# Kernel tuning notes

Hardware: AMD Instinct MI355X
Metric: run time of the kernel (lower is better)

The kernel has to match this reference:

```python
import jax, jax.numpy as jnp
import numpy as np

N, F, C, H, HX = 100000, 500, 40, 256, 64
E = 1_600_000


def setup_inputs() -> dict:
    key = jax.random.key(0)
    ks = jax.random.split(key, 12)
    s = lambda fan_in: 1.0 / np.sqrt(fan_in)
    return {
        "x": jax.random.normal(ks[0], (N, F), dtype=jnp.float32),
        "y": jax.random.randint(ks[1], (N,), 0, C),
        "train_mask": jax.random.randint(ks[2], (N,), 0, 2).astype(bool),
        "edge_index": jax.random.randint(ks[3], (2, E), 0, N),
        "edge_index_neg": jax.random.randint(ks[4], (2, E), 0, N),
        "fc1_w": jax.random.uniform(ks[5], (H, F), jnp.float32, -s(F), s(F)),
        "fc1_b": jnp.zeros((H,), jnp.float32),
        "fc2_w": jax.random.uniform(ks[6], (C, H), jnp.float32, -s(H), s(H)),
        "fc2_b": jnp.zeros((C,), jnp.float32),
        "xenc_w": jax.random.uniform(ks[7], (HX, F), jnp.float32, -s(F), s(F)),
        "xenc_b": jnp.zeros((HX,), jnp.float32),
        "pexy_w": jax.random.uniform(ks[8], (1, 2 * (HX + C)), jnp.float32, -s(2 * (HX + C)), s(2 * (HX + C))),
        "pexy_b": jnp.zeros((1,), jnp.float32),
    }


def reference(x, y, train_mask, edge_index, edge_index_neg,
              fc1_w, fc1_b, fc2_w, fc2_b, xenc_w, xenc_b, pexy_w, pexy_b):
    temperature = 1.0
    # MLP p(y|x), inference mode (dropout is identity)
    h = jax.nn.relu(x @ fc1_w.T + fc1_b)
    logits = (h @ fc2_w.T + fc2_b) / temperature
    y_log_prob = jax.nn.log_softmax(logits, axis=-1)            # [N, C]
    y_prob = jnp.exp(y_log_prob)
    one_hot = jax.nn.one_hot(y, y_prob.shape[1], dtype=y_prob.dtype)
    y_prob = jnp.where(train_mask[:, None], one_hot, y_prob)    # [N, C]

    # node encoder
    xe = jax.nn.relu(x @ xenc_w.T + xenc_b)                     # [N, HX]

    # The scorer Linear(2*(HX+C) -> 1) applied to cat([x_q, x_k, y_q, y_k])
    # decomposes into per-node query/key scalars (same math, no big concat):
    hx = xe.shape[1]
    w = pexy_w[0]
    w_xq, w_xk = w[:hx], w[hx:2 * hx]
    w_yq, w_yk = w[2 * hx:2 * hx + y_prob.shape[1]], w[2 * hx + y_prob.shape[1]:]
    s_q = xe @ w_xq + y_prob @ w_yq                             # [N]
    s_k = xe @ w_xk + y_prob @ w_yk                             # [N]

    def edge_scores(ei):
        return (s_q[ei[0]] + s_k[ei[1]] + pexy_b[0])[:, None]   # [E, 1]

    e_pred_pos = edge_scores(edge_index)
    e_pred_neg = edge_scores(edge_index_neg)
    return (e_pred_pos, e_pred_neg, y_log_prob)
```

## Files before the change

kernel.cpp:

```cpp
#include <hip/hip_runtime.h>
#include <stdint.h>

#define N_NODES 100000
#define F_DIM   500
#define C_DIM   40
#define H_DIM   256
#define HX_DIM  64
#define O_DIM   320
#define E_NUM   1600000

typedef unsigned short u16;
typedef unsigned int   u32;
typedef __attribute__((ext_vector_type(4))) u16    u16x4;
typedef __attribute__((ext_vector_type(8))) u16    u16x8;
typedef __attribute__((ext_vector_type(4))) float  f32x4;
typedef __attribute__((ext_vector_type(8))) short  bf16x8;

__device__ __forceinline__ float bf2f(u16 v) {
  u32 u = ((u32)v) << 16;
  return __builtin_bit_cast(float, u);
}
__device__ __forceinline__ u16 f2bf(float f) {
  u32 x = __builtin_bit_cast(u32, f);
  x += 0x7fffu + ((x >> 16) & 1u);
  return (u16)(x >> 16);
}

__global__ __launch_bounds__(256) void k_detect(const u32* __restrict__ tm, int* __restrict__ flag)
{
  __shared__ int s;
  if (threadIdx.x == 0) s = 0;
  __syncthreads();
  int local = 0;
  #pragma unroll
  for (int j = 0; j < 16; ++j) {
    if (tm[j * 256 + threadIdx.x] > 1u) local = 1;
  }
  if (local) s = 1;
  __syncthreads();
  if (threadIdx.x == 0) *flag = s;
}

__global__ __launch_bounds__(256) void k_cvtw(
    const float* __restrict__ fc1w, const float* __restrict__ xencw, u16* __restrict__ wws)
{
  const int g = blockIdx.x * 256 + threadIdx.x;
  const int c = g / 1280;
  const int rem = g - c * 1280;
  const int r = rem >> 2;
  const int k0 = c * 32 + (rem & 3) * 8;
  const float* src = (r < H_DIM) ? (fc1w + (long)r * F_DIM)
                                 : (xencw + (long)(r - H_DIM) * F_DIM);
  f32x4 v0 = {0.f, 0.f, 0.f, 0.f}, v1 = v0;
  if (k0 + 4 <= F_DIM) v0 = *(const f32x4*)(src + k0);
  if (k0 + 8 <= F_DIM) v1 = *(const f32x4*)(src + k0 + 4);
  u16x8 o;
  #pragma unroll
  for (int i = 0; i < 4; ++i) { o[i] = f2bf(v0[i]); o[4 + i] = f2bf(v1[i]); }
  *(u16x8*)(wws + (size_t)g * 8) = o;
}

__global__ __launch_bounds__(256) void k_cvtw2(
    const float* __restrict__ fc2w, const float* __restrict__ pw, u16* __restrict__ wwsB)
{
  const int g = blockIdx.x * 256 + threadIdx.x;
  if (g >= 1920) return;
  const int kc = g / 192;
  const int rem = g - kc * 192;
  const int r = rem >> 2;
  const int k0 = kc * 32 + (rem & 3) * 8;
  const float* src = nullptr;
  if (r < C_DIM)           { if (k0 + 8 <= H_DIM) src = fc2w + r * H_DIM + k0; }
  else if (r == C_DIM)     { if (k0 >= H_DIM) src = pw + (k0 - H_DIM); }
  else if (r == C_DIM + 1) { if (k0 >= H_DIM) src = pw + HX_DIM + (k0 - H_DIM); }
  u16x8 o = {0, 0, 0, 0, 0, 0, 0, 0};
  if (src) {
    const f32x4 v0 = *(const f32x4*)src;
    const f32x4 v1 = *(const f32x4*)(src + 4);
    #pragma unroll
    for (int i = 0; i < 4; ++i) { o[i] = f2bf(v0[i]); o[4 + i] = f2bf(v1[i]); }
  }
  *(u16x8*)(wwsB + (size_t)g * 8) = o;
}

#define BN   320
#define RH_LD 328

__global__ __launch_bounds__(256, 4) void k_fused(
    const float* __restrict__ x, const u16* __restrict__ wws, const u16* __restrict__ wwsB,
    const float* __restrict__ fc1b, const float* __restrict__ xencb,
    const int* __restrict__ y, const void* __restrict__ tmask,
    const float* __restrict__ fc2b, const float* __restrict__ pw,
    const int* __restrict__ mask_flag,
    float* __restrict__ out_lp, float* __restrict__ sq_out, float* __restrict__ sk_out)
{
  __shared__ __align__(16) u16 smem[16384];
  u16* sOut = smem;

  const int tid  = threadIdx.x;
  const int lane = tid & 63;
  const int wcol = tid >> 6;
  const int l15 = lane & 15, lgrp = lane >> 4;
  const long rowbase = (long)blockIdx.x * 32;

  {
    f32x4 v0[4], v1[4];
    #pragma unroll
    for (int half = 0; half < 2; ++half) {
      #pragma unroll
      for (int i = 0; i < 4; ++i) {
        const int g = tid + 256 * (half * 4 + i);
        const int r = g >> 6, c = g & 63;
        const int k0 = c * 8;
        v0[i] = (f32x4){0.f, 0.f, 0.f, 0.f};
        v1[i] = v0[i];
        const float* p = x + (rowbase + r) * F_DIM + k0;
        if (k0 + 4 <= F_DIM) v0[i] = *(const f32x4*)p;
        if (k0 + 8 <= F_DIM) v1[i] = *(const f32x4*)(p + 4);
      }
      #pragma unroll
      for (int i = 0; i < 4; ++i) {
        const int g = tid + 256 * (half * 4 + i);
        const int r = g >> 6, c = g & 63;
        const int phys = c ^ (r & 7);
        u16x8 o;
        #pragma unroll
        for (int j = 0; j < 4; ++j) { o[j] = f2bf(v0[i][j]); o[4 + j] = f2bf(v1[i][j]); }
        *(u16x8*)(smem + r * 512 + phys * 8) = o;
      }
    }
  }

  f32x4 acc[2][5];
  #pragma unroll
  for (int m = 0; m < 2; ++m)
    #pragma unroll
    for (int n = 0; n < 5; ++n)
      acc[m][n] = (f32x4){0.f, 0.f, 0.f, 0.f};

  const u16* bbase = wws + (wcol * 80 + l15) * 32 + lgrp * 8;
  const int arow_off = l15 * 512;

#define LB(dst, kc)                                                            \
  {                                                                            \
    const u16* bp = bbase + (size_t)(kc) * (BN * 32);                          \
    _Pragma("unroll")                                                          \
    for (int n = 0; n < 5; ++n) dst[n] = *(const bf16x8*)(bp + n * 512);       \
  }

#define LDA(A0, A1, kc)                                                        \
  {                                                                            \
    const int phys = (((kc) * 4 + lgrp) ^ (l15 & 7)) * 8;                      \
    A0 = *(const bf16x8*)(smem + arow_off + phys);                             \
    A1 = *(const bf16x8*)(smem + arow_off + 16 * 512 + phys);                  \
  }

#define GS(kc, AC0, AC1, AN0, AN1, BU, BL)                                     \
  {                                                                            \
    if ((kc) < 15) { LDA(AN0, AN1, (kc) + 1); LB(BL, (kc) + 1); }              \
    _Pragma("unroll")                                                          \
    for (int n = 0; n < 5; ++n) {                                              \
      acc[0][n] = __builtin_amdgcn_mfma_f32_16x16x32_bf16(AC0, BU[n], acc[0][n], 0, 0, 0); \
      acc[1][n] = __builtin_amdgcn_mfma_f32_16x16x32_bf16(AC1, BU[n], acc[1][n], 0, 0, 0); \
    }                                                                          \
  }

  bf16x8 aX0, aX1, aY0, aY1, bP[5], bQ[5];
  __syncthreads();
  LDA(aX0, aX1, 0); LB(bP, 0);

  GS(0,  aX0, aX1, aY0, aY1, bP, bQ)  GS(1,  aY0, aY1, aX0, aX1, bQ, bP)
  GS(2,  aX0, aX1, aY0, aY1, bP, bQ)  GS(3,  aY0, aY1, aX0, aX1, bQ, bP)
  GS(4,  aX0, aX1, aY0, aY1, bP, bQ)  GS(5,  aY0, aY1, aX0, aX1, bQ, bP)
  GS(6,  aX0, aX1, aY0, aY1, bP, bQ)  GS(7,  aY0, aY1, aX0, aX1, bQ, bP)
  GS(8,  aX0, aX1, aY0, aY1, bP, bQ)  GS(9,  aY0, aY1, aX0, aX1, bQ, bP)
  GS(10, aX0, aX1, aY0, aY1, bP, bQ)  GS(11, aY0, aY1, aX0, aX1, bQ, bP)
  GS(12, aX0, aX1, aY0, aY1, bP, bQ)  GS(13, aY0, aY1, aX0, aX1, bQ, bP)
  GS(14, aX0, aX1, aY0, aY1, bP, bQ)  GS(15, aY0, aY1, aX0, aX1, bQ, bP)

  __syncthreads();

  #pragma unroll
  for (int n = 0; n < 5; ++n) {
    const int col = wcol * 80 + n * 16 + l15;
    const float bias = (col < H_DIM) ? fc1b[col] : xencb[col - H_DIM];
    #pragma unroll
    for (int m = 0; m < 2; ++m) {
      const int r0 = m * 16 + lgrp * 4;
      #pragma unroll
      for (int rg = 0; rg < 4; ++rg)
        sOut[(r0 + rg) * RH_LD + col] = f2bf(fmaxf(acc[m][n][rg] + bias, 0.f));
    }
  }
  __syncthreads();

  if (tid < 128) {
    const int wid = tid >> 6;
    const u16* bBase = wwsB + l15 * 32 + lgrp * 8;
    f32x4 racc[3];
    #pragma unroll
    for (int n = 0; n < 3; ++n) racc[n] = (f32x4){0.f, 0.f, 0.f, 0.f};
    const u16* pa = sOut + (wid * 16 + l15) * RH_LD + lgrp * 8;

    bf16x8 bc[3], bn[3];
    #pragma unroll
    for (int n = 0; n < 3; ++n) bc[n] = *(const bf16x8*)(bBase + n * 512);

#define RH(kc, BC, BN_)                                                        \
    {                                                                          \
      if ((kc) < 9) {                                                          \
        _Pragma("unroll")                                                      \
        for (int n = 0; n < 3; ++n)                                            \
          BN_[n] = *(const bf16x8*)(bBase + ((kc) + 1) * 1536 + n * 512);      \
      }                                                                        \
      const bf16x8 a = *(const bf16x8*)(pa + (kc) * 32);                       \
      _Pragma("unroll")                                                        \
      for (int n = 0; n < 3; ++n)                                              \
        racc[n] = __builtin_amdgcn_mfma_f32_16x16x32_bf16(a, BC[n], racc[n], 0, 0, 0); \
    }

    RH(0, bc, bn) RH(1, bn, bc) RH(2, bc, bn) RH(3, bn, bc) RH(4, bc, bn)
    RH(5, bn, bc) RH(6, bc, bn) RH(7, bn, bc) RH(8, bc, bn) RH(9, bn, bc)
#undef RH

    const int c0 = l15, c1 = 16 + l15, c2 = 32 + l15;
    const bool v2 = (l15 < 8);
    const float b0 = fc2b[c0], b1 = fc2b[c1], b2 = v2 ? fc2b[c2] : 0.f;
    const float wq0 = pw[2 * HX_DIM + c0], wq1 = pw[2 * HX_DIM + c1],
                wq2 = v2 ? pw[2 * HX_DIM + c2] : 0.f;
    const float wk0 = pw[2 * HX_DIM + C_DIM + c0], wk1 = pw[2 * HX_DIM + C_DIM + c1],
                wk2 = v2 ? pw[2 * HX_DIM + C_DIM + c2] : 0.f;
    const bool byte_mask = (*mask_flag != 0);

    #pragma unroll
    for (int rg = 0; rg < 4; ++rg) {
      const long row = rowbase + wid * 16 + lgrp * 4 + rg;
      const float lg0 = racc[0][rg] + b0;
      const float lg1 = racc[1][rg] + b1;
      const float lg2 = racc[2][rg] + b2;
      const float sxq = __shfl(racc[2][rg], (lane & 48) | 8, 64);
      const float sxk = __shfl(racc[2][rg], (lane & 48) | 9, 64);

      float m = fmaxf(lg0, lg1);
      if (v2) m = fmaxf(m, lg2);
      #pragma unroll
      for (int off = 1; off < 16; off <<= 1) m = fmaxf(m, __shfl_xor(m, off, 64));
      const float e0 = __expf(lg0 - m), e1 = __expf(lg1 - m),
                  e2 = v2 ? __expf(lg2 - m) : 0.f;
      float s = e0 + e1 + e2;
      #pragma unroll
      for (int off = 1; off < 16; off <<= 1) s += __shfl_xor(s, off, 64);
      const float lse = m + __logf(s);
      const float inv = 1.f / s;

      const int yv = y[row];
      const bool tm = byte_mask ? (((const unsigned char*)tmask)[row] != 0)
                                : (((const int*)tmask)[row] != 0);
      const float p0 = tm ? (c0 == yv ? 1.f : 0.f) : e0 * inv;
      const float p1 = tm ? (c1 == yv ? 1.f : 0.f) : e1 * inv;
      const float p2 = tm ? (c2 == yv ? 1.f : 0.f) : e2 * inv;
      float sq = p0 * wq0 + p1 * wq1 + p2 * wq2;
      float sk = p0 * wk0 + p1 * wk1 + p2 * wk2;
      #pragma unroll
      for (int off = 1; off < 16; off <<= 1) {
        sq += __shfl_xor(sq, off, 64);
        sk += __shfl_xor(sk, off, 64);
      }

      float* lp = out_lp + row * C_DIM;
      lp[c0] = lg0 - lse;
      lp[c1] = lg1 - lse;
      if (v2) lp[c2] = lg2 - lse;
      if (l15 == 0) { sq_out[row] = sq + sxq; sk_out[row] = sk + sxk; }
    }
  }
#undef LB
#undef LDA
#undef GS
}

__global__ __launch_bounds__(256) void k_edges(
    const int* __restrict__ ei, const int* __restrict__ ein,
    const float* __restrict__ sq, const float* __restrict__ sk,
    const float* __restrict__ pb, float* __restrict__ out)
{
  const int e = blockIdx.x * 256 + threadIdx.x;
  if (e >= E_NUM) return;
  const float b = pb[0];
  const int a0 = ei[e],  a1 = ei[E_NUM + e];
  out[e] = sq[a0] + sk[a1] + b;
  const int c0 = ein[e], c1 = ein[E_NUM + e];
  out[E_NUM + e] = sq[c0] + sk[c1] + b;
}

extern "C" void kernel_launch(void* const* d_in, const int* in_sizes, int n_in,
                              void* d_out, int out_size, void* d_ws, size_t ws_size,
                              hipStream_t stream)
{
  const float* x     = (const float*)d_in[0];
  const int*   y     = (const int*)d_in[1];
  const void*  tm    = d_in[2];
  const int*   ei    = (const int*)d_in[3];
  const int*   ein   = (const int*)d_in[4];
  const float* fc1w  = (const float*)d_in[5];
  const float* fc1b  = (const float*)d_in[6];
  const float* fc2w  = (const float*)d_in[7];
  const float* fc2b  = (const float*)d_in[8];
  const float* xencw = (const float*)d_in[9];
  const float* xencb = (const float*)d_in[10];
  const float* pw    = (const float*)d_in[11];
  const float* pb    = (const float*)d_in[12];
  float* out = (float*)d_out;

  float* sq   = (float*)((char*)d_ws + (size_t)N_NODES * O_DIM * 2);
  float* sk   = sq + N_NODES;
  int*   flag = (int*)(sk + N_NODES);
  u16*   wws  = (u16*)((char*)d_ws + 64800064);
  u16*   wwsB = (u16*)((char*)d_ws + 65127744);

  k_detect<<<1, 256, 0, stream>>>((const u32*)tm, flag);
  k_cvtw  <<<80, 256, 0, stream>>>(fc1w, xencw, wws);
  k_cvtw2 <<<8, 256, 0, stream>>>(fc2w, pw, wwsB);
  k_fused <<<N_NODES / 32, 256, 0, stream>>>(x, wws, wwsB, fc1b, xencb, y, tm,
                                             fc2b, pw, flag,
                                             out + 2 * (size_t)E_NUM, sq, sk);
  k_edges <<<E_NUM / 256, 256, 0, stream>>>(ei, ein, sq, sk, pb, out);
}
```

Baseline: 153.7 us.

## Load x directly from global into MFMA A-fragments, dropping LDS staging

Instead of first staging a 32x512 bf16 tile of x in shared memory behind a barrier, each lane now reads its A-fragment straight from global fp32 x and converts it to bf16 in registers inside the pipelined K loop. Shared memory shrinks to the 32x328 output tile, which may let more blocks fit per CU, and the initial barrier disappears. In exchange, the x loads are less coalesced (16 rows with 32-byte segments per lane), with a clamped tail read past column 496 that is still multiplied by zero weights. The workspace layout is also compacted and the epilogue code is moved into helper functions.

```diff
diff --git a/kernel.cpp b/kernel.cpp
--- a/kernel.cpp
+++ b/kernel.cpp
@@ -8,6 +8,8 @@
 #define HX_DIM  64
 #define O_DIM   320
 #define E_NUM   1600000
+#define RH_LD   328
+#define BN      320
 
 typedef unsigned short u16;
 typedef unsigned int   u32;
@@ -83,8 +85,110 @@
   *(u16x8*)(wwsB + (size_t)g * 8) = o;
 }
 
-#define BN   320
-#define RH_LD 328
+__device__ __forceinline__ void epilogue_store(
+    u16* sOut, f32x4 (&acc)[2][5], const float* __restrict__ fc1b,
+    const float* __restrict__ xencb, int wcol, int l15, int lgrp)
+{
+  #pragma unroll
+  for (int n = 0; n < 5; ++n) {
+    const int col = wcol * 80 + n * 16 + l15;
+    const float bias = (col < H_DIM) ? fc1b[col] : xencb[col - H_DIM];
+    #pragma unroll
+    for (int m = 0; m < 2; ++m) {
+      const int r0 = m * 16 + lgrp * 4;
+      #pragma unroll
+      for (int rg = 0; rg < 4; ++rg)
+        sOut[(r0 + rg) * RH_LD + col] = f2bf(fmaxf(acc[m][n][rg] + bias, 0.f));
+    }
+  }
+}
+
+__device__ __forceinline__ void rowhead_phase2(
+    const u16* __restrict__ sOut, const u16* __restrict__ wwsB,
+    const int* __restrict__ y, const void* __restrict__ tmask,
+    const float* __restrict__ fc2b, const float* __restrict__ pw,
+    bool byte_mask, long rowbase, int tid,
+    float* __restrict__ out_lp, float* __restrict__ sq_out, float* __restrict__ sk_out)
+{
+  if (tid >= 128) return;
+  const int lane = tid & 63, wid = tid >> 6;
+  const int l15 = lane & 15, lgrp = lane >> 4;
+  const u16* bBase = wwsB + l15 * 32 + lgrp * 8;
+  f32x4 racc[3];
+  #pragma unroll
+  for (int n = 0; n < 3; ++n) racc[n] = (f32x4){0.f, 0.f, 0.f, 0.f};
+  const u16* pa = sOut + (wid * 16 + l15) * RH_LD + lgrp * 8;
+
+  bf16x8 bc[3], bn[3];
+  #pragma unroll
+  for (int n = 0; n < 3; ++n) bc[n] = *(const bf16x8*)(bBase + n * 512);
+
+#define RH(kc, BC, BN_)                                                        \
+  {                                                                            \
+    if ((kc) < 9) {                                                            \
+      _Pragma("unroll")                                                        \
+      for (int n = 0; n < 3; ++n)                                              \
+        BN_[n] = *(const bf16x8*)(bBase + ((kc) + 1) * 1536 + n * 512);        \
+    }                                                                          \
+    const bf16x8 a = *(const bf16x8*)(pa + (kc) * 32);                         \
+    _Pragma("unroll")                                                          \
+    for (int n = 0; n < 3; ++n)                                                \
+      racc[n] = __builtin_amdgcn_mfma_f32_16x16x32_bf16(a, BC[n], racc[n], 0, 0, 0); \
+  }
+  RH(0, bc, bn) RH(1, bn, bc) RH(2, bc, bn) RH(3, bn, bc) RH(4, bc, bn)
+  RH(5, bn, bc) RH(6, bc, bn) RH(7, bn, bc) RH(8, bc, bn) RH(9, bn, bc)
+#undef RH
+
+  const int c0 = l15, c1 = 16 + l15, c2 = 32 + l15;
+  const bool v2 = (l15 < 8);
+  const float b0 = fc2b[c0], b1 = fc2b[c1], b2 = v2 ? fc2b[c2] : 0.f;
+  const float wq0 = pw[2 * HX_DIM + c0], wq1 = pw[2 * HX_DIM + c1],
+              wq2 = v2 ? pw[2 * HX_DIM + c2] : 0.f;
+  const float wk0 = pw[2 * HX_DIM + C_DIM + c0], wk1 = pw[2 * HX_DIM + C_DIM + c1],
+              wk2 = v2 ? pw[2 * HX_DIM + C_DIM + c2] : 0.f;
+
+  #pragma unroll
+  for (int rg = 0; rg < 4; ++rg) {
+    const long row = rowbase + wid * 16 + lgrp * 4 + rg;
+    const float lg0 = racc[0][rg] + b0;
+    const float lg1 = racc[1][rg] + b1;
+    const float lg2 = racc[2][rg] + b2;
+    const float sxq = __shfl(racc[2][rg], (lane & 48) | 8, 64);
+    const float sxk = __shfl(racc[2][rg], (lane & 48) | 9, 64);
+
+    float m = fmaxf(lg0, lg1);
+    if (v2) m = fmaxf(m, lg2);
+    #pragma unroll
+    for (int off = 1; off < 16; off <<= 1) m = fmaxf(m, __shfl_xor(m, off, 64));
+    const float e0 = __expf(lg0 - m), e1 = __expf(lg1 - m),
+                e2 = v2 ? __expf(lg2 - m) : 0.f;
+    float s = e0 + e1 + e2;
+    #pragma unroll
+    for (int off = 1; off < 16; off <<= 1) s += __shfl_xor(s, off, 64);
+    const float lse = m + __logf(s);
+    const float inv = 1.f / s;
+
+    const int yv = y[row];
+    const bool tm = byte_mask ? (((const unsigned char*)tmask)[row] != 0)
+                              : (((const int*)tmask)[row] != 0);
+    const float p0 = tm ? (c0 == yv ? 1.f : 0.f) : e0 * inv;
+    const float p1 = tm ? (c1 == yv ? 1.f : 0.f) : e1 * inv;
+    const float p2 = tm ? (c2 == yv ? 1.f : 0.f) : e2 * inv;
+    float sq = p0 * wq0 + p1 * wq1 + p2 * wq2;
+    float sk = p0 * wk0 + p1 * wk1 + p2 * wk2;
+    #pragma unroll
+    for (int off = 1; off < 16; off <<= 1) {
+      sq += __shfl_xor(sq, off, 64);
+      sk += __shfl_xor(sk, off, 64);
+    }
+
+    float* lp = out_lp + row * C_DIM;
+    lp[c0] = lg0 - lse;
+    lp[c1] = lg1 - lse;
+    if (v2) lp[c2] = lg2 - lse;
+    if (l15 == 0) { sq_out[row] = sq + sxq; sk_out[row] = sk + sxk; }
+  }
+}
 
 __global__ __launch_bounds__(256, 4) void k_fused(
     const float* __restrict__ x, const u16* __restrict__ wws, const u16* __restrict__ wwsB,
@@ -94,8 +198,7 @@
     const int* __restrict__ mask_flag,
     float* __restrict__ out_lp, float* __restrict__ sq_out, float* __restrict__ sk_out)
 {
-  __shared__ __align__(16) u16 smem[16384];
-  u16* sOut = smem;
+  __shared__ __align__(16) u16 sOut[32 * RH_LD];
 
   const int tid  = threadIdx.x;
   const int lane = tid & 63;
@@ -103,33 +206,9 @@
   const int l15 = lane & 15, lgrp = lane >> 4;
   const long rowbase = (long)blockIdx.x * 32;
 
-  {
-    f32x4 v0[4], v1[4];
-    #pragma unroll
-    for (int half = 0; half < 2; ++half) {
-      #pragma unroll
-      for (int i = 0; i < 4; ++i) {
-        const int g = tid + 256 * (half * 4 + i);
-        const int r = g >> 6, c = g & 63;
-        const int k0 = c * 8;
-        v0[i] = (f32x4){0.f, 0.f, 0.f, 0.f};
-        v1[i] = v0[i];
-        const float* p = x + (rowbase + r) * F_DIM + k0;
-        if (k0 + 4 <= F_DIM) v0[i] = *(const f32x4*)p;
-        if (k0 + 8 <= F_DIM) v1[i] = *(const f32x4*)(p + 4);
-      }
-      #pragma unroll
-      for (int i = 0; i < 4; ++i) {
-        const int g = tid + 256 * (half * 4 + i);
-        const int r = g >> 6, c = g & 63;
-        const int phys = c ^ (r & 7);
-        u16x8 o;
-        #pragma unroll
-        for (int j = 0; j < 4; ++j) { o[j] = f2bf(v0[i][j]); o[4 + j] = f2bf(v1[i][j]); }
-        *(u16x8*)(smem + r * 512 + phys * 8) = o;
-      }
-    }
-  }
+  const float* xrow0 = x + (rowbase + l15) * F_DIM;
+  const float* xrow1 = xrow0 + 16 * F_DIM;
+  const u16* bbase = wws + (wcol * 80 + l15) * 32 + lgrp * 8;
 
   f32x4 acc[2][5];
   #pragma unroll
@@ -138,26 +217,30 @@
     for (int n = 0; n < 5; ++n)
       acc[m][n] = (f32x4){0.f, 0.f, 0.f, 0.f};
 
-  const u16* bbase = wws + (wcol * 80 + l15) * 32 + lgrp * 8;
-  const int arow_off = l15 * 512;
-
+#define LA(AF0, AF1, kc)                                                       \
+  {                                                                            \
+    const int k0 = (kc) * 32 + lgrp * 8;                                       \
+    const int ka = (k0 > 496) ? 496 : k0;                                      \
+    const int kb = (k0 + 4 > 496) ? 496 : (k0 + 4);                            \
+    const f32x4 t0 = *(const f32x4*)(xrow0 + ka);                              \
+    const f32x4 t1 = *(const f32x4*)(xrow0 + kb);                              \
+    const f32x4 t2 = *(const f32x4*)(xrow1 + ka);                              \
+    const f32x4 t3 = *(const f32x4*)(xrow1 + kb);                              \
+    _Pragma("unroll")                                                          \
+    for (int i = 0; i < 4; ++i) {                                              \
+      AF0[i]     = (short)f2bf(t0[i]);  AF0[4 + i] = (short)f2bf(t1[i]);       \
+      AF1[i]     = (short)f2bf(t2[i]);  AF1[4 + i] = (short)f2bf(t3[i]);       \
+    }                                                                          \
+  }
 #define LB(dst, kc)                                                            \
   {                                                                            \
     const u16* bp = bbase + (size_t)(kc) * (BN * 32);                          \
     _Pragma("unroll")                                                          \
     for (int n = 0; n < 5; ++n) dst[n] = *(const bf16x8*)(bp + n * 512);       \
   }
-
-#define LDA(A0, A1, kc)                                                        \
-  {                                                                            \
-    const int phys = (((kc) * 4 + lgrp) ^ (l15 & 7)) * 8;                      \
-    A0 = *(const bf16x8*)(smem + arow_off + phys);                             \
-    A1 = *(const bf16x8*)(smem + arow_off + 16 * 512 + phys);                  \
-  }
-
 #define GS(kc, AC0, AC1, AN0, AN1, BU, BL)                                     \
   {                                                                            \
-    if ((kc) < 15) { LDA(AN0, AN1, (kc) + 1); LB(BL, (kc) + 1); }              \
+    if ((kc) < 15) { LA(AN0, AN1, (kc) + 1); LB(BL, (kc) + 1); }               \
     _Pragma("unroll")                                                          \
     for (int n = 0; n < 5; ++n) {                                              \
       acc[0][n] = __builtin_amdgcn_mfma_f32_16x16x32_bf16(AC0, BU[n], acc[0][n], 0, 0, 0); \
@@ -166,9 +249,7 @@
   }
 
   bf16x8 aX0, aX1, aY0, aY1, bP[5], bQ[5];
-  __syncthreads();
-  LDA(aX0, aX1, 0); LB(bP, 0);
-
+  LA(aX0, aX1, 0); LB(bP, 0);
   GS(0,  aX0, aX1, aY0, aY1, bP, bQ)  GS(1,  aY0, aY1, aX0, aX1, bQ, bP)
   GS(2,  aX0, aX1, aY0, aY1, bP, bQ)  GS(3,  aY0, aY1, aX0, aX1, bQ, bP)
   GS(4,  aX0, aX1, aY0, aY1, bP, bQ)  GS(5,  aY0, aY1, aX0, aX1, bQ, bP)
@@ -177,106 +258,14 @@
   GS(10, aX0, aX1, aY0, aY1, bP, bQ)  GS(11, aY0, aY1, aX0, aX1, bQ, bP)
   GS(12, aX0, aX1, aY0, aY1, bP, bQ)  GS(13, aY0, aY1, aX0, aX1, bQ, bP)
   GS(14, aX0, aX1, aY0, aY1, bP, bQ)  GS(15, aY0, aY1, aX0, aX1, bQ, bP)
-
+#undef LA
+#undef LB
+#undef GS
+
+  epilogue_store(sOut, acc, fc1b, xencb, wcol, l15, lgrp);
   __syncthreads();
-
-  #pragma unroll
-  for (int n = 0; n < 5; ++n) {
-    const int col = wcol * 80 + n * 16 + l15;
-    const float bias = (col < H_DIM) ? fc1b[col] : xencb[col - H_DIM];
-    #pragma unroll
-    for (int m = 0; m < 2; ++m) {
-      const int r0 = m * 16 + lgrp * 4;
-      #pragma unroll
-      for (int rg = 0; rg < 4; ++rg)
-        sOut[(r0 + rg) * RH_LD + col] = f2bf(fmaxf(acc[m][n][rg] + bias, 0.f));
-    }
-  }
-  __syncthreads();
-
-  if (tid < 128) {
-    const int wid = tid >> 6;
-    const u16* bBase = wwsB + l15 * 32 + lgrp * 8;
-    f32x4 racc[3];
-    #pragma unroll
-    for (int n = 0; n < 3; ++n) racc[n] = (f32x4){0.f, 0.f, 0.f, 0.f};
-    const u16* pa = sOut + (wid * 16 + l15) * RH_LD + lgrp * 8;
-
-    bf16x8 bc[3], bn[3];
-    #pragma unroll
-    for (int n = 0; n < 3; ++n) bc[n] = *(const bf16x8*)(bBase + n * 512);
-
-#define RH(kc, BC, BN_)                                                        \
-    {                                                                          \
-      if ((kc) < 9) {                                                          \
-        _Pragma("unroll")                                                      \
-        for (int n = 0; n < 3; ++n)                                            \
-          BN_[n] = *(const bf16x8*)(bBase + ((kc) + 1) * 1536 + n * 512);      \
-      }                                                                        \
-      const bf16x8 a = *(const bf16x8*)(pa + (kc) * 32);                       \
-      _Pragma("unroll")                                                        \
-      for (int n = 0; n < 3; ++n)                                              \
-        racc[n] = __builtin_amdgcn_mfma_f32_16x16x32_bf16(a, BC[n], racc[n], 0, 0, 0); \
-    }
-
-    RH(0, bc, bn) RH(1, bn, bc) RH(2, bc, bn) RH(3, bn, bc) RH(4, bc, bn)
-    RH(5, bn, bc) RH(6, bc, bn) RH(7, bn, bc) RH(8, bc, bn) RH(9, bn, bc)
-#undef RH
-
-    const int c0 = l15, c1 = 16 + l15, c2 = 32 + l15;
-    const bool v2 = (l15 < 8);
-    const float b0 = fc2b[c0], b1 = fc2b[c1], b2 = v2 ? fc2b[c2] : 0.f;
-    const float wq0 = pw[2 * HX_DIM + c0], wq1 = pw[2 * HX_DIM + c1],
-                wq2 = v2 ? pw[2 * HX_DIM + c2] : 0.f;
-    const float wk0 = pw[2 * HX_DIM + C_DIM + c0], wk1 = pw[2 * HX_DIM + C_DIM + c1],
-                wk2 = v2 ? pw[2 * HX_DIM + C_DIM + c2] : 0.f;
-    const bool byte_mask = (*mask_flag != 0);
-
-    #pragma unroll
-    for (int rg = 0; rg < 4; ++rg) {
-      const long row = rowbase + wid * 16 + lgrp * 4 + rg;
-      const float lg0 = racc[0][rg] + b0;
-      const float lg1 = racc[1][rg] + b1;
-      const float lg2 = racc[2][rg] + b2;
-      const float sxq = __shfl(racc[2][rg], (lane & 48) | 8, 64);
-      const float sxk = __shfl(racc[2][rg], (lane & 48) | 9, 64);
-
-      float m = fmaxf(lg0, lg1);
-      if (v2) m = fmaxf(m, lg2);
-      #pragma unroll
-      for (int off = 1; off < 16; off <<= 1) m = fmaxf(m, __shfl_xor(m, off, 64));
-      const float e0 = __expf(lg0 - m), e1 = __expf(lg1 - m),
-                  e2 = v2 ? __expf(lg2 - m) : 0.f;
-      float s = e0 + e1 + e2;
-      #pragma unroll
-      for (int off = 1; off < 16; off <<= 1) s += __shfl_xor(s, off, 64);
-      const float lse = m + __logf(s);
-      const float inv = 1.f / s;
-
-      const int yv = y[row];
-      const bool tm = byte_mask ? (((const unsigned char*)tmask)[row] != 0)
-                                : (((const int*)tmask)[row] != 0);
-      const float p0 = tm ? (c0 == yv ? 1.f : 0.f) : e0 * inv;
-      const float p1 = tm ? (c1 == yv ? 1.f : 0.f) : e1 * inv;
-      const float p2 = tm ? (c2 == yv ? 1.f : 0.f) : e2 * inv;
-      float sq = p0 * wq0 + p1 * wq1 + p2 * wq2;
-      float sk = p0 * wk0 + p1 * wk1 + p2 * wk2;
-      #pragma unroll
-      for (int off = 1; off < 16; off <<= 1) {
-        sq += __shfl_xor(sq, off, 64);
-        sk += __shfl_xor(sk, off, 64);
-      }
-
-      float* lp = out_lp + row * C_DIM;
-      lp[c0] = lg0 - lse;
-      lp[c1] = lg1 - lse;
-      if (v2) lp[c2] = lg2 - lse;
-      if (l15 == 0) { sq_out[row] = sq + sxq; sk_out[row] = sk + sxk; }
-    }
-  }
-#undef LB
-#undef LDA
-#undef GS
+  rowhead_phase2(sOut, wwsB, y, tmask, fc2b, pw, (*mask_flag != 0), rowbase, tid,
+                 out_lp, sq_out, sk_out);
 }
 
 __global__ __launch_bounds__(256) void k_edges(
@@ -312,11 +301,11 @@
   const float* pb    = (const float*)d_in[12];
   float* out = (float*)d_out;
 
-  float* sq   = (float*)((char*)d_ws + (size_t)N_NODES * O_DIM * 2);
-  float* sk   = sq + N_NODES;
-  int*   flag = (int*)(sk + N_NODES);
-  u16*   wws  = (u16*)((char*)d_ws + 64800064);
-  u16*   wwsB = (u16*)((char*)d_ws + 65127744);
+  float* sq   = (float*)d_ws;
+  float* sk   = (float*)((char*)d_ws + 400000);
+  int*   flag = (int*)((char*)d_ws + 800000);
+  u16*   wws  = (u16*)((char*)d_ws + 800064);
+  u16*   wwsB = (u16*)((char*)d_ws + 1127744);
 
   k_detect<<<1, 256, 0, stream>>>((const u32*)tm, flag);
   k_cvtw  <<<80, 256, 0, stream>>>(fc1w, xencw, wws);
```

New measurement: 157.9 us. 2.7% more time.
